# Kernel optimization log

Hardware: AMD Instinct MI355X
Metric: run time of the kernel (lower is better)

The kernel has to match this reference:

```python
import jax, jax.numpy as jnp
import numpy as np

B, S, DIN, DSLOT, NHEADS = 1024, 1024, 128, 64, 2
TEMPERATURE = 1.0


def setup_inputs() -> dict:
    key = jax.random.key(0)
    ks = jax.random.split(key, 7)
    slot_feats = jax.random.normal(ks[0], (B, S, DIN), dtype=jnp.float32)
    slot_mask = jax.random.uniform(ks[1], (B, S), dtype=jnp.float32)
    # slot_mlp: Linear(DIN, DSLOT) -> ReLU -> Linear(DSLOT, DSLOT)
    W1 = jax.random.normal(ks[2], (DIN, DSLOT), dtype=jnp.float32) * (1.0 / np.sqrt(DIN))
    b1 = jnp.zeros((DSLOT,), dtype=jnp.float32)
    W2 = jax.random.normal(ks[3], (DSLOT, DSLOT), dtype=jnp.float32) * (1.0 / np.sqrt(DSLOT))
    b2 = jnp.zeros((DSLOT,), dtype=jnp.float32)
    q = jax.random.normal(ks[4], (NHEADS, DSLOT), dtype=jnp.float32) * 0.1
    return {"slot_feats": slot_feats, "slot_mask": slot_mask,
            "W1": W1, "b1": b1, "W2": W2, "b2": b2, "q": q, "k": 8}


def reference(slot_feats, slot_mask, W1, b1, W2, b2, q, k):
    d_slot = W2.shape[-1]
    # slot MLP embed: [B,S,Dslot]
    H = jnp.maximum(slot_feats @ W1 + b1, 0.0) @ W2 + b2
    scale = 1.0 / jnp.sqrt(jnp.asarray(d_slot, dtype=H.dtype))
    # per-head score, averaged over heads: [B,S]
    scores = jnp.einsum('bsd,hd->bsh', H, q).mean(axis=-1) * scale
    mask = slot_mask > 0.5
    scores_masked = jnp.where(mask, scores, -jnp.inf)
    all_masked = ~jnp.any(mask, axis=1)  # [B]
    temp = max(TEMPERATURE, 1e-6)
    sm_in = jnp.where(all_masked[:, None], jnp.zeros_like(scores), scores_masked) / temp
    attnW = jax.nn.softmax(sm_in, axis=1)  # [B,S]
    ctx = jnp.einsum('bs,bsd->bd', attnW, H)  # use_soft_ctx=True
    # top-k on raw masked scores (eval: no gumbel)
    k_eff = min(k, scores.shape[1])
    invalid_rows = jnp.all(jnp.isinf(scores_masked), axis=1)
    safe_scores = jnp.where(invalid_rows[:, None], jnp.zeros_like(scores_masked), scores_masked)
    _, topk_idx = jax.lax.top_k(safe_scores, k_eff)  # [B,k]
    sel = jnp.take_along_axis(H, topk_idx[:, :, None], axis=1)  # [B,k,Dslot]
    return sel, ctx, attnW
```

## Files before the change

kernel.cpp:

```cpp
#include <hip/hip_runtime.h>
#include <hip/hip_bf16.h>

#define BB 1024
#define SS 1024
#define DIN 128
#define DSLOT 64
#define TOPK 8
#define TOKENS (BB*SS)
#define TM 128

__device__ __forceinline__ unsigned short f2bf(float x) {
    unsigned u = __float_as_uint(x);
    return (unsigned short)((u + 0x7fffu + ((u >> 16) & 1u)) >> 16);
}
__device__ __forceinline__ float bf2f(unsigned u16) {
    return __uint_as_float(u16 << 16);
}

__global__ void prep_kernel(const float* __restrict__ W2, const float* __restrict__ b2,
                            const float* __restrict__ q, float* __restrict__ vv) {
    __shared__ float qm[64];
    int d = threadIdx.x;
    if (d < 64) qm[d] = (q[d] + q[64 + d]) * 0.0625f;
    __syncthreads();
    if (d < 64) {
        float acc = 0.f;
        #pragma unroll
        for (int j = 0; j < 64; ++j) acc = fmaf(W2[d * 64 + j], qm[j], acc);
        vv[d] = acc;
    }
    if (d == 0) {
        float c = 0.f;
        for (int j = 0; j < 64; ++j) c = fmaf(b2[j], qm[j], c);
        vv[64] = c;
    }
}

__global__ __launch_bounds__(256) void mlp_kernel(
    const float* __restrict__ feats, const float* __restrict__ W1,
    const float* __restrict__ b1, const float* __restrict__ W2,
    const float* __restrict__ b2, const float* __restrict__ vv,
    unsigned short* __restrict__ Hws, float* __restrict__ scores)
{
    __shared__ float Xs[TM][33];
    __shared__ unsigned short Hs[TM][66];
    __shared__ float W1s[32][64];
    __shared__ float W2s[64][64];
    __shared__ float vS[64], b1s[64], b2s[64];
    __shared__ float c0s;

    const int tid = threadIdx.x;
    const int tx = tid & 3;
    const int ty = tid >> 2;
    const int d0 = tx * 16;
    const long t0 = (long)blockIdx.x * TM;

    for (int i = tid; i < 64 * 64; i += 256) W2s[i >> 6][i & 63] = W2[i];
    if (tid < 64) { vS[tid] = vv[tid]; b1s[tid] = b1[tid]; b2s[tid] = b2[tid]; }
    if (tid == 0) c0s = vv[64];

    float acc1[2][16];
    #pragma unroll
    for (int t = 0; t < 2; ++t)
        #pragma unroll
        for (int j = 0; j < 16; ++j) acc1[t][j] = 0.f;

    for (int kc = 0; kc < 4; ++kc) {
        __syncthreads();
        #pragma unroll
        for (int i = 0; i < 4; ++i) {
            int li = tid + i * 256;
            int row = li >> 3, c4 = li & 7;
            float4 f = *(const float4*)&feats[(t0 + row) * DIN + kc * 32 + c4 * 4];
            Xs[row][c4 * 4 + 0] = f.x; Xs[row][c4 * 4 + 1] = f.y;
            Xs[row][c4 * 4 + 2] = f.z; Xs[row][c4 * 4 + 3] = f.w;
        }
        #pragma unroll
        for (int i = 0; i < 2; ++i) {
            int li = tid + i * 256;
            int row = li >> 4, c4 = li & 15;
            *(float4*)&W1s[row][c4 * 4] = *(const float4*)&W1[(kc * 32 + row) * DSLOT + c4 * 4];
        }
        __syncthreads();
        #pragma unroll 8
        for (int kk = 0; kk < 32; ++kk) {
            float w[16];
            *(float4*)&w[0]  = *(const float4*)&W1s[kk][d0];
            *(float4*)&w[4]  = *(const float4*)&W1s[kk][d0 + 4];
            *(float4*)&w[8]  = *(const float4*)&W1s[kk][d0 + 8];
            *(float4*)&w[12] = *(const float4*)&W1s[kk][d0 + 12];
            float x0 = Xs[2 * ty + 0][kk];
            float x1 = Xs[2 * ty + 1][kk];
            #pragma unroll
            for (int j = 0; j < 16; ++j) {
                acc1[0][j] = fmaf(x0, w[j], acc1[0][j]);
                acc1[1][j] = fmaf(x1, w[j], acc1[1][j]);
            }
        }
    }

    float h[2][16];
    #pragma unroll
    for (int t = 0; t < 2; ++t)
        #pragma unroll
        for (int j = 0; j < 16; ++j) h[t][j] = fmaxf(acc1[t][j] + b1s[d0 + j], 0.f);

    float p0 = 0.f, p1 = 0.f;
    #pragma unroll
    for (int j = 0; j < 16; ++j) {
        p0 = fmaf(h[0][j], vS[d0 + j], p0);
        p1 = fmaf(h[1][j], vS[d0 + j], p1);
    }
    p0 += __shfl_xor(p0, 1); p0 += __shfl_xor(p0, 2);
    p1 += __shfl_xor(p1, 1); p1 += __shfl_xor(p1, 2);
    if (tx == 0) {
        scores[t0 + 2 * ty + 0] = p0 + c0s;
        scores[t0 + 2 * ty + 1] = p1 + c0s;
    }

    #pragma unroll
    for (int t = 0; t < 2; ++t)
        #pragma unroll
        for (int j = 0; j < 8; ++j) {
            unsigned pk = (unsigned)f2bf(h[t][2 * j]) | ((unsigned)f2bf(h[t][2 * j + 1]) << 16);
            *(unsigned*)&Hs[2 * ty + t][d0 + 2 * j] = pk;
        }
    __syncthreads();

    float acc2[2][16];
    #pragma unroll
    for (int t = 0; t < 2; ++t)
        #pragma unroll
        for (int j = 0; j < 16; ++j) acc2[t][j] = b2s[d0 + j];

    #pragma unroll 8
    for (int kk = 0; kk < 64; ++kk) {
        float w[16];
        *(float4*)&w[0]  = *(const float4*)&W2s[kk][d0];
        *(float4*)&w[4]  = *(const float4*)&W2s[kk][d0 + 4];
        *(float4*)&w[8]  = *(const float4*)&W2s[kk][d0 + 8];
        *(float4*)&w[12] = *(const float4*)&W2s[kk][d0 + 12];
        float x0 = bf2f(Hs[2 * ty + 0][kk]);
        float x1 = bf2f(Hs[2 * ty + 1][kk]);
        #pragma unroll
        for (int j = 0; j < 16; ++j) {
            acc2[0][j] = fmaf(x0, w[j], acc2[0][j]);
            acc2[1][j] = fmaf(x1, w[j], acc2[1][j]);
        }
    }

    #pragma unroll
    for (int t = 0; t < 2; ++t) {
        unsigned hw[8];
        #pragma unroll
        for (int j = 0; j < 8; ++j)
            hw[j] = (unsigned)f2bf(acc2[t][2 * j]) | ((unsigned)f2bf(acc2[t][2 * j + 1]) << 16);
        unsigned* dst = (unsigned*)&Hws[(t0 + 2 * ty + t) * DSLOT + d0];
        *(uint4*)dst = make_uint4(hw[0], hw[1], hw[2], hw[3]);
        *((uint4*)dst + 1) = make_uint4(hw[4], hw[5], hw[6], hw[7]);
    }
}

__global__ __launch_bounds__(256) void attn_kernel(
    const float* __restrict__ scores, const float* __restrict__ mask,
    const unsigned short* __restrict__ Hws,
    float* __restrict__ out_sel, float* __restrict__ out_ctx, float* __restrict__ out_attn)
{
    const int b = blockIdx.x, tid = threadIdx.x;
    __shared__ float sc[SS];
    __shared__ float ex[SS];
    __shared__ float red[256];
    __shared__ int   redi[256];
    __shared__ unsigned char used[SS];
    __shared__ int anyValid;
    __shared__ int selIdx[TOPK];

    if (tid == 0) anyValid = 0;
    __syncthreads();

    const float* srow = scores + (long)b * SS;
    const float* mrow = mask + (long)b * SS;
    int localAny = 0;
    #pragma unroll
    for (int k = 0; k < 4; ++k) {
        int i = tid + k * 256;
        bool valid = mrow[i] > 0.5f;
        sc[i] = valid ? srow[i] : -__builtin_inff();
        used[i] = 0;
        if (valid) localAny = 1;
    }
    if (localAny) atomicOr(&anyValid, 1);
    __syncthreads();
    const int av = anyValid;

    float mloc = -__builtin_inff();
    #pragma unroll
    for (int k = 0; k < 4; ++k) {
        int i = tid + k * 256;
        mloc = fmaxf(mloc, av ? sc[i] : 0.f);
    }
    red[tid] = mloc; __syncthreads();
    for (int s = 128; s > 0; s >>= 1) {
        if (tid < s) red[tid] = fmaxf(red[tid], red[tid + s]);
        __syncthreads();
    }
    const float M = red[0];
    __syncthreads();

    float sloc = 0.f;
    #pragma unroll
    for (int k = 0; k < 4; ++k) {
        int i = tid + k * 256;
        float v = av ? sc[i] : 0.f;
        float e = expf(v - M);
        ex[i] = e; sloc += e;
    }
    red[tid] = sloc; __syncthreads();
    for (int s = 128; s > 0; s >>= 1) {
        if (tid < s) red[tid] += red[tid + s];
        __syncthreads();
    }
    const float invZ = 1.f / red[0];
    __syncthreads();
    #pragma unroll
    for (int k = 0; k < 4; ++k) {
        int i = tid + k * 256;
        float w = ex[i] * invZ;
        ex[i] = w;
        out_attn[(long)b * SS + i] = w;
    }

    for (int r = 0; r < TOPK; ++r) {
        float bv = -__builtin_inff(); int bi = SS;
        #pragma unroll
        for (int k = 0; k < 4; ++k) {
            int i = tid + k * 256;
            if (!used[i]) {
                float v = av ? sc[i] : 0.f;
                if (v > bv || (v == bv && i < bi)) { bv = v; bi = i; }
            }
        }
        red[tid] = bv; redi[tid] = bi; __syncthreads();
        for (int s = 128; s > 0; s >>= 1) {
            if (tid < s) {
                float v2 = red[tid + s]; int i2 = redi[tid + s];
                if (v2 > red[tid] || (v2 == red[tid] && i2 < redi[tid])) {
                    red[tid] = v2; redi[tid] = i2;
                }
            }
            __syncthreads();
        }
        if (tid == 0) { selIdx[r] = redi[0]; used[redi[0]] = 1; }
        __syncthreads();
    }

    for (int f = tid; f < TOPK * DSLOT; f += 256) {
        int r = f >> 6, d = f & 63;
        unsigned short hb = Hws[((long)b * SS + selIdx[r]) * DSLOT + d];
        out_sel[(long)b * (TOPK * DSLOT) + f] = bf2f(hb);
    }

    const int dg = tid & 15, sg = tid >> 4;
    float a0 = 0.f, a1 = 0.f, a2 = 0.f, a3 = 0.f;
    #pragma unroll 4
    for (int it = 0; it < 64; ++it) {
        int s = sg * 64 + it;
        uint2 u = *(const uint2*)&Hws[((long)b * SS + s) * DSLOT + dg * 4];
        float w = ex[s];
        a0 = fmaf(w, bf2f(u.x & 0xffffu), a0);
        a1 = fmaf(w, bf2f(u.x >> 16), a1);
        a2 = fmaf(w, bf2f(u.y & 0xffffu), a2);
        a3 = fmaf(w, bf2f(u.y >> 16), a3);
    }
    __syncthreads();
    sc[sg * 64 + dg * 4 + 0] = a0;
    sc[sg * 64 + dg * 4 + 1] = a1;
    sc[sg * 64 + dg * 4 + 2] = a2;
    sc[sg * 64 + dg * 4 + 3] = a3;
    __syncthreads();
    if (tid < 64) {
        float acc = 0.f;
        #pragma unroll
        for (int g = 0; g < 16; ++g) acc += sc[g * 64 + tid];
        out_ctx[(long)b * DSLOT + tid] = acc;
    }
}

extern "C" void kernel_launch(void* const* d_in, const int* in_sizes, int n_in,
                              void* d_out, int out_size, void* d_ws, size_t ws_size,
                              hipStream_t stream) {
    (void)in_sizes; (void)n_in; (void)out_size; (void)ws_size;
    const float* feats = (const float*)d_in[0];
    const float* smask = (const float*)d_in[1];
    const float* W1 = (const float*)d_in[2];
    const float* b1 = (const float*)d_in[3];
    const float* W2 = (const float*)d_in[4];
    const float* b2 = (const float*)d_in[5];
    const float* q  = (const float*)d_in[6];

    char* ws = (char*)d_ws;
    unsigned short* Hws = (unsigned short*)ws;
    float* scores = (float*)(ws + (size_t)TOKENS * DSLOT * 2);
    float* vv = (float*)(ws + (size_t)TOKENS * DSLOT * 2 + (size_t)TOKENS * 4);

    float* out_sel  = (float*)d_out;
    float* out_ctx  = out_sel + (long)BB * TOPK * DSLOT;
    float* out_attn = out_ctx + (long)BB * DSLOT;

    prep_kernel<<<1, 64, 0, stream>>>(W2, b2, q, vv);
    mlp_kernel<<<TOKENS / TM, 256, 0, stream>>>(feats, W1, b1, W2, b2, vv, Hws, scores);
    attn_kernel<<<BB, 256, 0, stream>>>(scores, smask, Hws, out_sel, out_ctx, out_attn);
}
```

Baseline: 1.019 ms.

## Restructure MLP to one token per thread and use wave-shuffle reductions in attention

The MLP kernel now gives each thread a full token row, with 64 accumulators, and reads W1/W2 straight from global memory as wave-uniform broadcast loads instead of staging them in shared memory. The shared buffer is reused to hold the hidden activations and to stage a coalesced write of H. The attention kernel replaces the shared-memory tree reductions with wave shuffles plus ballot, and runs top-k on packed 64-bit keys that hold the score and index. The aim is fewer LDS round trips and barriers, at the cost of heavy register pressure (128 accumulators live across the phases) and reliance on scalar/global caching for the weights.

```diff
diff --git a/kernel.cpp b/kernel.cpp
--- a/kernel.cpp
+++ b/kernel.cpp
@@ -7,7 +7,6 @@
 #define DSLOT 64
 #define TOPK 8
 #define TOKENS (BB*SS)
-#define TM 128
 
 __device__ __forceinline__ unsigned short f2bf(float x) {
     unsigned u = __float_as_uint(x);
@@ -36,221 +35,192 @@
     }
 }
 
-__global__ __launch_bounds__(256) void mlp_kernel(
+__global__ __launch_bounds__(256, 4) void mlp_kernel(
     const float* __restrict__ feats, const float* __restrict__ W1,
     const float* __restrict__ b1, const float* __restrict__ W2,
     const float* __restrict__ b2, const float* __restrict__ vv,
     unsigned short* __restrict__ Hws, float* __restrict__ scores)
 {
-    __shared__ float Xs[TM][33];
-    __shared__ unsigned short Hs[TM][66];
-    __shared__ float W1s[32][64];
-    __shared__ float W2s[64][64];
-    __shared__ float vS[64], b1s[64], b2s[64];
-    __shared__ float c0s;
+    __shared__ float Xs[256][33];
+    unsigned* Hp = (unsigned*)&Xs[0][0];
 
     const int tid = threadIdx.x;
-    const int tx = tid & 3;
-    const int ty = tid >> 2;
-    const int d0 = tx * 16;
-    const long t0 = (long)blockIdx.x * TM;
-
-    for (int i = tid; i < 64 * 64; i += 256) W2s[i >> 6][i & 63] = W2[i];
-    if (tid < 64) { vS[tid] = vv[tid]; b1s[tid] = b1[tid]; b2s[tid] = b2[tid]; }
-    if (tid == 0) c0s = vv[64];
-
-    float acc1[2][16];
-    #pragma unroll
-    for (int t = 0; t < 2; ++t)
-        #pragma unroll
-        for (int j = 0; j < 16; ++j) acc1[t][j] = 0.f;
-
+    const long t0 = (long)blockIdx.x * 256;
+
+    float acc[64];
+    #pragma unroll
+    for (int j = 0; j < 64; ++j) acc[j] = 0.f;
+
+    #pragma unroll 1
     for (int kc = 0; kc < 4; ++kc) {
         __syncthreads();
         #pragma unroll
-        for (int i = 0; i < 4; ++i) {
+        for (int i = 0; i < 8; ++i) {
             int li = tid + i * 256;
             int row = li >> 3, c4 = li & 7;
             float4 f = *(const float4*)&feats[(t0 + row) * DIN + kc * 32 + c4 * 4];
             Xs[row][c4 * 4 + 0] = f.x; Xs[row][c4 * 4 + 1] = f.y;
             Xs[row][c4 * 4 + 2] = f.z; Xs[row][c4 * 4 + 3] = f.w;
         }
-        #pragma unroll
-        for (int i = 0; i < 2; ++i) {
-            int li = tid + i * 256;
-            int row = li >> 4, c4 = li & 15;
-            *(float4*)&W1s[row][c4 * 4] = *(const float4*)&W1[(kc * 32 + row) * DSLOT + c4 * 4];
-        }
-        __syncthreads();
-        #pragma unroll 8
-        for (int kk = 0; kk < 32; ++kk) {
-            float w[16];
-            *(float4*)&w[0]  = *(const float4*)&W1s[kk][d0];
-            *(float4*)&w[4]  = *(const float4*)&W1s[kk][d0 + 4];
-            *(float4*)&w[8]  = *(const float4*)&W1s[kk][d0 + 8];
-            *(float4*)&w[12] = *(const float4*)&W1s[kk][d0 + 12];
-            float x0 = Xs[2 * ty + 0][kk];
-            float x1 = Xs[2 * ty + 1][kk];
+        __syncthreads();
+        #pragma unroll 1
+        for (int kq = 0; kq < 8; ++kq) {
+            float x0 = Xs[tid][kq * 4 + 0];
+            float x1 = Xs[tid][kq * 4 + 1];
+            float x2 = Xs[tid][kq * 4 + 2];
+            float x3 = Xs[tid][kq * 4 + 3];
+            const int kk = kc * 32 + kq * 4;
+            const float* w0 = W1 + (kk + 0) * DSLOT;
+            const float* w1 = W1 + (kk + 1) * DSLOT;
+            const float* w2 = W1 + (kk + 2) * DSLOT;
+            const float* w3 = W1 + (kk + 3) * DSLOT;
             #pragma unroll
-            for (int j = 0; j < 16; ++j) {
-                acc1[0][j] = fmaf(x0, w[j], acc1[0][j]);
-                acc1[1][j] = fmaf(x1, w[j], acc1[1][j]);
+            for (int j = 0; j < 64; ++j) {
+                acc[j] = fmaf(x0, w0[j], acc[j]);
+                acc[j] = fmaf(x1, w1[j], acc[j]);
+                acc[j] = fmaf(x2, w2[j], acc[j]);
+                acc[j] = fmaf(x3, w3[j], acc[j]);
             }
         }
     }
 
-    float h[2][16];
-    #pragma unroll
-    for (int t = 0; t < 2; ++t)
-        #pragma unroll
-        for (int j = 0; j < 16; ++j) h[t][j] = fmaxf(acc1[t][j] + b1s[d0 + j], 0.f);
-
-    float p0 = 0.f, p1 = 0.f;
-    #pragma unroll
-    for (int j = 0; j < 16; ++j) {
-        p0 = fmaf(h[0][j], vS[d0 + j], p0);
-        p1 = fmaf(h[1][j], vS[d0 + j], p1);
-    }
-    p0 += __shfl_xor(p0, 1); p0 += __shfl_xor(p0, 2);
-    p1 += __shfl_xor(p1, 1); p1 += __shfl_xor(p1, 2);
-    if (tx == 0) {
-        scores[t0 + 2 * ty + 0] = p0 + c0s;
-        scores[t0 + 2 * ty + 1] = p1 + c0s;
-    }
-
-    #pragma unroll
-    for (int t = 0; t < 2; ++t)
-        #pragma unroll
-        for (int j = 0; j < 8; ++j) {
-            unsigned pk = (unsigned)f2bf(h[t][2 * j]) | ((unsigned)f2bf(h[t][2 * j + 1]) << 16);
-            *(unsigned*)&Hs[2 * ty + t][d0 + 2 * j] = pk;
-        }
-    __syncthreads();
-
-    float acc2[2][16];
-    #pragma unroll
-    for (int t = 0; t < 2; ++t)
-        #pragma unroll
-        for (int j = 0; j < 16; ++j) acc2[t][j] = b2s[d0 + j];
-
-    #pragma unroll 8
-    for (int kk = 0; kk < 64; ++kk) {
-        float w[16];
-        *(float4*)&w[0]  = *(const float4*)&W2s[kk][d0];
-        *(float4*)&w[4]  = *(const float4*)&W2s[kk][d0 + 4];
-        *(float4*)&w[8]  = *(const float4*)&W2s[kk][d0 + 8];
-        *(float4*)&w[12] = *(const float4*)&W2s[kk][d0 + 12];
-        float x0 = bf2f(Hs[2 * ty + 0][kk]);
-        float x1 = bf2f(Hs[2 * ty + 1][kk]);
-        #pragma unroll
-        for (int j = 0; j < 16; ++j) {
-            acc2[0][j] = fmaf(x0, w[j], acc2[0][j]);
-            acc2[1][j] = fmaf(x1, w[j], acc2[1][j]);
-        }
-    }
-
-    #pragma unroll
-    for (int t = 0; t < 2; ++t) {
-        unsigned hw[8];
-        #pragma unroll
-        for (int j = 0; j < 8; ++j)
-            hw[j] = (unsigned)f2bf(acc2[t][2 * j]) | ((unsigned)f2bf(acc2[t][2 * j + 1]) << 16);
-        unsigned* dst = (unsigned*)&Hws[(t0 + 2 * ty + t) * DSLOT + d0];
-        *(uint4*)dst = make_uint4(hw[0], hw[1], hw[2], hw[3]);
-        *((uint4*)dst + 1) = make_uint4(hw[4], hw[5], hw[6], hw[7]);
-    }
-}
-
-__global__ __launch_bounds__(256) void attn_kernel(
+    float score = 0.f;
+    #pragma unroll
+    for (int j2 = 0; j2 < 32; ++j2) {
+        float h0 = fmaxf(acc[2 * j2 + 0] + b1[2 * j2 + 0], 0.f);
+        float h1 = fmaxf(acc[2 * j2 + 1] + b1[2 * j2 + 1], 0.f);
+        score = fmaf(h0, vv[2 * j2 + 0], score);
+        score = fmaf(h1, vv[2 * j2 + 1], score);
+        Hp[tid * 33 + j2] = (unsigned)f2bf(h0) | ((unsigned)f2bf(h1) << 16);
+    }
+    scores[t0 + tid] = score + vv[64];
+
+    float acc2[64];
+    #pragma unroll
+    for (int j = 0; j < 64; ++j) acc2[j] = b2[j];
+
+    #pragma unroll 1
+    for (int kq = 0; kq < 16; ++kq) {
+        unsigned p0 = Hp[tid * 33 + kq * 2 + 0];
+        unsigned p1 = Hp[tid * 33 + kq * 2 + 1];
+        float h0 = bf2f(p0 & 0xffffu), h1 = bf2f(p0 >> 16);
+        float h2 = bf2f(p1 & 0xffffu), h3 = bf2f(p1 >> 16);
+        const int kk = kq * 4;
+        const float* w0 = W2 + (kk + 0) * DSLOT;
+        const float* w1 = W2 + (kk + 1) * DSLOT;
+        const float* w2 = W2 + (kk + 2) * DSLOT;
+        const float* w3 = W2 + (kk + 3) * DSLOT;
+        #pragma unroll
+        for (int j = 0; j < 64; ++j) {
+            acc2[j] = fmaf(h0, w0[j], acc2[j]);
+            acc2[j] = fmaf(h1, w1[j], acc2[j]);
+            acc2[j] = fmaf(h2, w2[j], acc2[j]);
+            acc2[j] = fmaf(h3, w3[j], acc2[j]);
+        }
+    }
+
+    #pragma unroll
+    for (int j2 = 0; j2 < 32; ++j2)
+        Hp[tid * 33 + j2] = (unsigned)f2bf(acc2[2 * j2 + 0]) | ((unsigned)f2bf(acc2[2 * j2 + 1]) << 16);
+    __syncthreads();
+
+    uint2* dst = (uint2*)(Hws + t0 * DSLOT);
+    #pragma unroll
+    for (int i = 0; i < 16; ++i) {
+        int g0 = (tid + i * 256) * 2;
+        int r = g0 >> 5, c = g0 & 31;
+        dst[tid + i * 256] = make_uint2(Hp[r * 33 + c], Hp[r * 33 + c + 1]);
+    }
+}
+
+__global__ __launch_bounds__(256, 4) void attn_kernel(
     const float* __restrict__ scores, const float* __restrict__ mask,
     const unsigned short* __restrict__ Hws,
     float* __restrict__ out_sel, float* __restrict__ out_ctx, float* __restrict__ out_attn)
 {
     const int b = blockIdx.x, tid = threadIdx.x;
-    __shared__ float sc[SS];
+    const int lane = tid & 63, wave = tid >> 6;
     __shared__ float ex[SS];
-    __shared__ float red[256];
-    __shared__ int   redi[256];
-    __shared__ unsigned char used[SS];
-    __shared__ int anyValid;
+    __shared__ float cred[SS];
+    __shared__ float wred[4];
+    __shared__ unsigned long long kred[4];
     __shared__ int selIdx[TOPK];
-
-    if (tid == 0) anyValid = 0;
-    __syncthreads();
 
     const float* srow = scores + (long)b * SS;
     const float* mrow = mask + (long)b * SS;
-    int localAny = 0;
+
+    float sv[4]; bool any = false;
     #pragma unroll
     for (int k = 0; k < 4; ++k) {
         int i = tid + k * 256;
-        bool valid = mrow[i] > 0.5f;
-        sc[i] = valid ? srow[i] : -__builtin_inff();
-        used[i] = 0;
-        if (valid) localAny = 1;
-    }
-    if (localAny) atomicOr(&anyValid, 1);
-    __syncthreads();
-    const int av = anyValid;
-
-    float mloc = -__builtin_inff();
+        bool v = mrow[i] > 0.5f;
+        sv[k] = v ? srow[i] : -__builtin_inff();
+        any |= v;
+    }
+    unsigned long long ball = __ballot(any);
+    if (lane == 0) kred[wave] = ball;
+    __syncthreads();
+    const bool av = (kred[0] | kred[1] | kred[2] | kred[3]) != 0ULL;
+
+    float eff[4];
+    #pragma unroll
+    for (int k = 0; k < 4; ++k) eff[k] = av ? sv[k] : 0.f;
+
+    float m = fmaxf(fmaxf(eff[0], eff[1]), fmaxf(eff[2], eff[3]));
+    #pragma unroll
+    for (int off = 32; off > 0; off >>= 1) m = fmaxf(m, __shfl_xor(m, off));
+    __syncthreads();
+    if (lane == 0) wred[wave] = m;
+    __syncthreads();
+    const float M = fmaxf(fmaxf(wred[0], wred[1]), fmaxf(wred[2], wred[3]));
+
+    float e[4]; float s = 0.f;
+    #pragma unroll
+    for (int k = 0; k < 4; ++k) { e[k] = expf(eff[k] - M); s += e[k]; }
+    #pragma unroll
+    for (int off = 32; off > 0; off >>= 1) s += __shfl_xor(s, off);
+    __syncthreads();
+    if (lane == 0) wred[wave] = s;
+    __syncthreads();
+    const float invZ = 1.f / (wred[0] + wred[1] + wred[2] + wred[3]);
+
     #pragma unroll
     for (int k = 0; k < 4; ++k) {
         int i = tid + k * 256;
-        mloc = fmaxf(mloc, av ? sc[i] : 0.f);
-    }
-    red[tid] = mloc; __syncthreads();
-    for (int s = 128; s > 0; s >>= 1) {
-        if (tid < s) red[tid] = fmaxf(red[tid], red[tid + s]);
-        __syncthreads();
-    }
-    const float M = red[0];
-    __syncthreads();
-
-    float sloc = 0.f;
+        float w = e[k] * invZ;
+        ex[i] = w;
+        out_attn[(long)b * SS + i] = w;
+    }
+
+    unsigned long long key[4];
     #pragma unroll
     for (int k = 0; k < 4; ++k) {
         int i = tid + k * 256;
-        float v = av ? sc[i] : 0.f;
-        float e = expf(v - M);
-        ex[i] = e; sloc += e;
-    }
-    red[tid] = sloc; __syncthreads();
-    for (int s = 128; s > 0; s >>= 1) {
-        if (tid < s) red[tid] += red[tid + s];
-        __syncthreads();
-    }
-    const float invZ = 1.f / red[0];
-    __syncthreads();
-    #pragma unroll
-    for (int k = 0; k < 4; ++k) {
-        int i = tid + k * 256;
-        float w = ex[i] * invZ;
-        ex[i] = w;
-        out_attn[(long)b * SS + i] = w;
-    }
-
+        unsigned ub = __float_as_uint(eff[k]);
+        ub = (ub & 0x80000000u) ? ~ub : (ub | 0x80000000u);
+        key[k] = ((unsigned long long)ub << 32) | (unsigned)(SS - 1 - i);
+    }
     for (int r = 0; r < TOPK; ++r) {
-        float bv = -__builtin_inff(); int bi = SS;
-        #pragma unroll
-        for (int k = 0; k < 4; ++k) {
-            int i = tid + k * 256;
-            if (!used[i]) {
-                float v = av ? sc[i] : 0.f;
-                if (v > bv || (v == bv && i < bi)) { bv = v; bi = i; }
-            }
-        }
-        red[tid] = bv; redi[tid] = bi; __syncthreads();
-        for (int s = 128; s > 0; s >>= 1) {
-            if (tid < s) {
-                float v2 = red[tid + s]; int i2 = redi[tid + s];
-                if (v2 > red[tid] || (v2 == red[tid] && i2 < redi[tid])) {
-                    red[tid] = v2; redi[tid] = i2;
-                }
-            }
-            __syncthreads();
-        }
-        if (tid == 0) { selIdx[r] = redi[0]; used[redi[0]] = 1; }
+        unsigned long long kmax = key[0];
+        if (key[1] > kmax) kmax = key[1];
+        if (key[2] > kmax) kmax = key[2];
+        if (key[3] > kmax) kmax = key[3];
+        #pragma unroll
+        for (int off = 32; off > 0; off >>= 1) {
+            unsigned long long o = __shfl_xor(kmax, off);
+            if (o > kmax) kmax = o;
+        }
+        if (lane == 0) kred[wave] = kmax;
+        __syncthreads();
+        unsigned long long kb = kred[0];
+        if (kred[1] > kb) kb = kred[1];
+        if (kred[2] > kb) kb = kred[2];
+        if (kred[3] > kb) kb = kred[3];
+        int idx = (SS - 1) - (int)(kb & 0xffffffffu);
+        if (tid == 0) selIdx[r] = idx;
+        #pragma unroll
+        for (int k = 0; k < 4; ++k)
+            if (tid + k * 256 == idx) key[k] = 0ULL;
         __syncthreads();
     }
 
@@ -264,25 +234,24 @@
     float a0 = 0.f, a1 = 0.f, a2 = 0.f, a3 = 0.f;
     #pragma unroll 4
     for (int it = 0; it < 64; ++it) {
-        int s = sg * 64 + it;
-        uint2 u = *(const uint2*)&Hws[((long)b * SS + s) * DSLOT + dg * 4];
-        float w = ex[s];
+        int s2 = sg * 64 + it;
+        uint2 u = *(const uint2*)&Hws[((long)b * SS + s2) * DSLOT + dg * 4];
+        float w = ex[s2];
         a0 = fmaf(w, bf2f(u.x & 0xffffu), a0);
         a1 = fmaf(w, bf2f(u.x >> 16), a1);
         a2 = fmaf(w, bf2f(u.y & 0xffffu), a2);
         a3 = fmaf(w, bf2f(u.y >> 16), a3);
     }
-    __syncthreads();
-    sc[sg * 64 + dg * 4 + 0] = a0;
-    sc[sg * 64 + dg * 4 + 1] = a1;
-    sc[sg * 64 + dg * 4 + 2] = a2;
-    sc[sg * 64 + dg * 4 + 3] = a3;
+    cred[sg * 64 + dg * 4 + 0] = a0;
+    cred[sg * 64 + dg * 4 + 1] = a1;
+    cred[sg * 64 + dg * 4 + 2] = a2;
+    cred[sg * 64 + dg * 4 + 3] = a3;
     __syncthreads();
     if (tid < 64) {
-        float acc = 0.f;
-        #pragma unroll
-        for (int g = 0; g < 16; ++g) acc += sc[g * 64 + tid];
-        out_ctx[(long)b * DSLOT + tid] = acc;
+        float accc = 0.f;
+        #pragma unroll
+        for (int g = 0; g < 16; ++g) accc += cred[g * 64 + tid];
+        out_ctx[(long)b * DSLOT + tid] = accc;
     }
 }
 
@@ -308,6 +277,6 @@
     float* out_attn = out_ctx + (long)BB * DSLOT;
 
     prep_kernel<<<1, 64, 0, stream>>>(W2, b2, q, vv);
-    mlp_kernel<<<TOKENS / TM, 256, 0, stream>>>(feats, W1, b1, W2, b2, vv, Hws, scores);
+    mlp_kernel<<<TOKENS / 256, 256, 0, stream>>>(feats, W1, b1, W2, b2, vv, Hws, scores);
     attn_kernel<<<BB, 256, 0, stream>>>(scores, smask, Hws, out_sel, out_ctx, out_attn);
 }
```

Result: slower. 1.045 ms (+2.6%).
